# Optimization experiments

Measured on AMD Instinct MI355X. Metric: run time of the kernel, lower is better.

## Reference

```python
import jax, jax.numpy as jnp
import numpy as np

S = 72
IMG_W, IMG_H = 640, 360
STRIDE = 32
FMAP_H, FMAP_W = IMG_H // STRIDE, IMG_W // STRIDE  # 11, 20
N_OFFSETS = S
N_STRIPS = S - 1
ANGLES = np.array([15.0, 22.0, 30.0, 39.0, 49.0, 60.0, 72.0, 80.0, 90.0, 100.0, 108.0, 120.0, 131.0, 141.0, 150.0, 158.0, 165.0])
N_ANG = 17
N_PRED = 2 + 2 + 1 + N_OFFSETS  # 77
N_EDGE = FMAP_W + 2 * FMAP_H    # 42
N_PROP = N_ANG * N_EDGE         # 714
NMS_THRES = 15.0
BACKBONE_C = 512
CONV_C = 1024


def _make_anchors():
    anchor_ys = np.linspace(1.0, 0.0, N_OFFSETS)
    tan = np.tan(np.deg2rad(ANGLES))
    def side(origins):
        out = np.zeros((N_ANG, N_PRED, len(origins)), np.float32)
        for i, (sx, sy) in enumerate(origins):
            out[:, 2, i] = 1.0 - sy
            out[:, 3, i] = sx
            out[:, 5:, i] = (sx + (sy - anchor_ys)[None, :] / tan[:, None]) * IMG_W
        return out.reshape(N_ANG * N_PRED, len(origins))
    left = side([(0.0, y) for y in np.linspace(1.0, 0.0, FMAP_H)])
    right = side([(1.0, y) for y in np.linspace(1.0, 0.0, FMAP_H)])
    bottom = side([(x, 1.0) for x in np.linspace(1.0, 0.0, FMAP_W)])
    anchors = np.zeros((N_ANG * N_PRED, FMAP_H, FMAP_W), np.float32)
    anchors[:, :, 0] = left
    anchors[:, :, -1] = right
    anchors[:, -1, :] = bottom
    edge = np.concatenate([anchors[:, :, 0], anchors[:, :, -1], anchors[:, -1, :]], 1)  # [1309,42]
    anch_dim = edge.reshape(N_ANG, N_PRED, N_EDGE).transpose(2, 0, 1).reshape(N_PROP, N_PRED)
    return jnp.asarray(anchors), jnp.asarray(anch_dim)


def setup_inputs():
    key = jax.random.key(0)
    ks = jax.random.split(key, 4)
    B = 32
    feat = jax.random.normal(ks[0], (B, BACKBONE_C, FMAP_H, FMAP_W), jnp.float32)
    W_conv = jax.random.normal(ks[1], (CONV_C, BACKBONE_C), jnp.float32) * 0.02
    b_conv = jnp.zeros((CONV_C,), jnp.float32)
    W_cls = jax.random.normal(ks[2], (2 * N_ANG, CONV_C), jnp.float32) * 0.02
    b_cls = jnp.zeros((2 * N_ANG,), jnp.float32)
    W_reg = jax.random.normal(ks[3], (N_ANG * (N_OFFSETS + 1), CONV_C), jnp.float32) * 0.02
    b_reg = jnp.zeros((N_ANG * (N_OFFSETS + 1),), jnp.float32)
    anchors, anchors_anchor_dim = _make_anchors()
    return {"feat": feat, "W_conv": W_conv, "b_conv": b_conv, "W_cls": W_cls, "b_cls": b_cls,
            "W_reg": W_reg, "b_reg": b_reg, "anchors": anchors, "anchors_anchor_dim": anchors_anchor_dim}


def _proposals(feat, W_conv, b_conv, W_cls, b_cls, W_reg, b_reg, anchors):
    B = feat.shape[0]
    features = jnp.einsum('bchw,oc->bohw', feat, W_conv) + b_conv[None, :, None, None]
    cls_f = jnp.einsum('bchw,oc->bohw', features, W_cls) + b_cls[None, :, None, None]
    reg_f = jnp.einsum('bchw,oc->bohw', features, W_reg) + b_reg[None, :, None, None]
    anch = anchors.reshape(N_ANG, N_PRED, FMAP_H, FMAP_W)
    cls_r = cls_f.reshape(B, N_ANG, 2, FMAP_H, FMAP_W)
    reg_r = reg_f.reshape(B, N_ANG, N_OFFSETS + 1, FMAP_H, FMAP_W)
    # slots 0:2 <- cls logits (set), slots 2:4 <- anchor (copied), slots 4: <- anchor + reg
    mid = jnp.broadcast_to(anch[None, :, 2:4], (B, N_ANG, 2, FMAP_H, FMAP_W))
    tail = anch[None, :, 4:] + reg_r
    lane = jnp.concatenate([cls_r, mid, tail], axis=2)  # [B,17,77,h,w]
    # gather the three feature-map edges: left col, right col, bottom row
    edges = jnp.concatenate([lane[:, :, :, :, 0], lane[:, :, :, :, -1], lane[:, :, :, -1, :]], axis=3)  # [B,17,77,42]
    return edges.transpose(0, 3, 1, 2).reshape(B, N_PROP, N_PRED)  # [B,714,77]


def _nms_one(props, scores):
    # greedy line-NMS over proposals of one image, shapes static
    order = jnp.argsort(-scores)
    p = props[order]
    start = jnp.clip(jnp.round(p[:, 2] * N_STRIPS), 0.0, float(N_STRIPS))
    end = jnp.clip(start + p[:, 4] - 1.0, 0.0, float(N_STRIPS))
    xs = p[:, 5:]  # [N,72]
    s = jnp.maximum(start[:, None], start[None, :])
    e = jnp.minimum(end[:, None], end[None, :])
    idx = jnp.arange(N_OFFSETS, dtype=p.dtype)
    m = (idx[None, None, :] >= s[..., None]) & (idx[None, None, :] <= e[..., None])  # [N,N,72]
    diff = jnp.abs(xs[:, None, :] - xs[None, :, :])  # [N,N,72]
    cnt = e - s + 1.0
    dist = jnp.where(cnt > 0, jnp.sum(diff * m, -1) / jnp.maximum(cnt, 1.0), jnp.inf)
    sup = dist < NMS_THRES
    n = p.shape[0]
    pos = jnp.arange(n)
    def step(suppressed, i):
        keep_i = ~suppressed[i]
        suppressed = suppressed | (keep_i & sup[i] & (pos > i))
        return suppressed, keep_i
    _, keep_sorted = jax.lax.scan(step, jnp.zeros(n, bool), pos)
    return jnp.zeros(n, bool).at[order].set(keep_sorted)


def reference(feat, W_conv, b_conv, W_cls, b_cls, W_reg, b_reg, anchors, anchors_anchor_dim):
    proposals = _proposals(feat, W_conv, b_conv, W_cls, b_cls, W_reg, b_reg, anchors)
    scores = jax.nn.softmax(proposals[..., :2], axis=-1)[..., 1]  # [B,714]
    keep_mask = jax.lax.map(lambda pr: _nms_one(pr[0], pr[1]), (proposals, scores))  # [B,714]
    return proposals, keep_mask, scores
```

## Files before the change

kernel.cpp:

```cpp
#include <hip/hip_runtime.h>
#include <math.h>

#define NB     32
#define FH     11
#define FW     20
#define CIN    512
#define CMID   1024
#define NANG   17
#define NPREDD 77
#define NEDGE  42
#define NPROPP 714
#define NOFF   72
#define NCLS   34
#define NREGR  1241
#define N2PAD  1280
#define MTOT   1344
#define NSTRIPSF 71.0f
#define PADK   40

typedef unsigned long long u64;
typedef unsigned short ushortt;
typedef short s8v __attribute__((ext_vector_type(8)));
typedef ushortt u4v __attribute__((ext_vector_type(4)));
typedef float f4v __attribute__((ext_vector_type(4)));

__device__ inline ushortt f2bf(float f) {
    unsigned u = __float_as_uint(f);
    u += 0x7fffu + ((u >> 16) & 1u);
    return (ushortt)(u >> 16);
}
__device__ inline float bf2f(ushortt h) {
    return __uint_as_float(((unsigned)h) << 16);
}

__global__ __launch_bounds__(256) void k_prep(const float* __restrict__ feat,
                                              ushortt* __restrict__ A1hi,
                                              ushortt* __restrict__ A1lo,
                                              const float* __restrict__ Wconv,
                                              ushortt* __restrict__ B1h,
                                              ushortt* __restrict__ B1l,
                                              const float* __restrict__ Wcls,
                                              const float* __restrict__ Wreg,
                                              ushortt* __restrict__ B2h,
                                              ushortt* __restrict__ B2l,
                                              const float* __restrict__ AD,
                                              float* __restrict__ outP,
                                              float* __restrict__ kst)
{
    int bid = blockIdx.x, tid = threadIdx.x;
    if (bid < 2688) {
        int idx = bid * 256 + tid;
        int m = idx >> 9, c = idx & 511;
        int b = m / NEDGE, e = m - b * NEDGE;
        int h, w;
        if (e < FH)          { h = e;      w = 0;      }
        else if (e < 2 * FH) { h = e - FH; w = FW - 1; }
        else                 { h = FH - 1; w = e - 2 * FH; }
        float v = feat[((size_t)(b * CIN + c) * FH + h) * FW + w];
        ushortt hi = f2bf(v);
        A1hi[idx] = hi;
        A1lo[idx] = f2bf(v - bf2f(hi));
    } else if (bid < 2688 + 512) {
        int t = (bid - 2688) * 256 + tid;
        float4 v = *(const float4*)(Wconv + (size_t)t * 4);
        float vf[4] = {v.x, v.y, v.z, v.w};
        u4v hv, lv;
#pragma unroll
        for (int j = 0; j < 4; ++j) {
            ushortt h = f2bf(vf[j]);
            hv[j] = h;
            lv[j] = f2bf(vf[j] - bf2f(h));
        }
        *(u4v*)(B1h + (size_t)t * 4) = hv;
        *(u4v*)(B1l + (size_t)t * 4) = lv;
    } else if (bid < 4480) {
        int t = (bid - 3200) * 256 + tid;
        int row = t >> 8, col = (t & 255) * 4;
        float4 v = make_float4(0.f, 0.f, 0.f, 0.f);
        if (row < NCLS)              v = *(const float4*)(Wcls + (size_t)row * CMID + col);
        else if (row < NCLS + NREGR) v = *(const float4*)(Wreg + (size_t)(row - NCLS) * CMID + col);
        float vf[4] = {v.x, v.y, v.z, v.w};
        u4v hv, lv;
#pragma unroll
        for (int j = 0; j < 4; ++j) {
            ushortt h = f2bf(vf[j]);
            hv[j] = h;
            lv[j] = f2bf(vf[j] - bf2f(h));
        }
        *(u4v*)(B2h + (size_t)t * 4) = hv;
        *(u4v*)(B2l + (size_t)t * 4) = lv;
    } else if (bid < 4659) {
        int idx = (bid - 4480) * 256 + tid;
        if (idx < NB * NPROPP * 2) {
            int bp = idx >> 1;
            int p = 2 + (idx & 1);
            int prop = bp - (bp / NPROPP) * NPROPP;
            outP[(size_t)bp * NPREDD + p] = AD[prop * NPREDD + p];
        }
    } else {
        if (tid < NPROPP) {
            float p2 = AD[tid * NPREDD + 2];
            kst[tid] = fminf(fmaxf(rintf(p2 * NSTRIPSF), 0.0f), NSTRIPSF);
        }
    }
}

__global__ __launch_bounds__(256) void k_gemm1m(const ushortt* __restrict__ Ahi,
                                                const ushortt* __restrict__ Alo,
                                                const ushortt* __restrict__ Bh,
                                                const ushortt* __restrict__ Bl,
                                                const float* __restrict__ bias,
                                                ushortt* __restrict__ Chi,
                                                ushortt* __restrict__ Clo)
{
    const int K = CIN, N = CMID;
    __shared__ __align__(16) ushortt Ash[2][64 * PADK], Asl[2][64 * PADK];
    __shared__ __align__(16) ushortt Bsh[2][64 * PADK], Bsl[2][64 * PADK];
    int tid = threadIdx.x;
    int m0 = blockIdx.y * 64, n0 = blockIdx.x * 64;
    int srow = tid >> 2, sg = tid & 3;
    int lane = tid & 63, wv = tid >> 6;
    int wm = (wv & 1) * 32, wn = (wv >> 1) * 32;
    int quad = lane >> 4, l15 = lane & 15;
    int wo = srow * PADK + sg * 8;

    f4v acc[2][2];
#pragma unroll
    for (int i = 0; i < 2; ++i)
#pragma unroll
        for (int j = 0; j < 2; ++j) acc[i][j] = (f4v){0.f, 0.f, 0.f, 0.f};

    const ushortt* Ahp = Ahi + (size_t)(m0 + srow) * K + sg * 8;
    const ushortt* Alp = Alo + (size_t)(m0 + srow) * K + sg * 8;
    const ushortt* Bhp = Bh  + (size_t)(n0 + srow) * K + sg * 8;
    const ushortt* Blp = Bl  + (size_t)(n0 + srow) * K + sg * 8;

    s8v ra = *(const s8v*)Ahp;
    s8v rl = *(const s8v*)Alp;
    s8v rb = *(const s8v*)Bhp;
    s8v rc = *(const s8v*)Blp;
    *(s8v*)&Ash[0][wo] = ra;
    *(s8v*)&Asl[0][wo] = rl;
    *(s8v*)&Bsh[0][wo] = rb;
    *(s8v*)&Bsl[0][wo] = rc;
    __syncthreads();

    int buf = 0;
    for (int k0 = 0; k0 < K; k0 += 32) {
        bool more = (k0 + 32 < K);
        if (more) {
            ra = *(const s8v*)(Ahp + k0 + 32);
            rl = *(const s8v*)(Alp + k0 + 32);
            rb = *(const s8v*)(Bhp + k0 + 32);
            rc = *(const s8v*)(Blp + k0 + 32);
        }
        s8v ah[2], al[2], bh[2], bl[2];
#pragma unroll
        for (int s = 0; s < 2; ++s) {
            ah[s] = *(const s8v*)&Ash[buf][(wm + s * 16 + l15) * PADK + quad * 8];
            al[s] = *(const s8v*)&Asl[buf][(wm + s * 16 + l15) * PADK + quad * 8];
            bh[s] = *(const s8v*)&Bsh[buf][(wn + s * 16 + l15) * PADK + quad * 8];
            bl[s] = *(const s8v*)&Bsl[buf][(wn + s * 16 + l15) * PADK + quad * 8];
        }
#pragma unroll
        for (int sm = 0; sm < 2; ++sm)
#pragma unroll
            for (int sn = 0; sn < 2; ++sn) {
                acc[sm][sn] = __builtin_amdgcn_mfma_f32_16x16x32_bf16(al[sm], bh[sn], acc[sm][sn], 0, 0, 0);
                acc[sm][sn] = __builtin_amdgcn_mfma_f32_16x16x32_bf16(ah[sm], bl[sn], acc[sm][sn], 0, 0, 0);
                acc[sm][sn] = __builtin_amdgcn_mfma_f32_16x16x32_bf16(ah[sm], bh[sn], acc[sm][sn], 0, 0, 0);
            }
        if (more) {
            *(s8v*)&Ash[buf ^ 1][wo] = ra;
            *(s8v*)&Asl[buf ^ 1][wo] = rl;
            *(s8v*)&Bsh[buf ^ 1][wo] = rb;
            *(s8v*)&Bsl[buf ^ 1][wo] = rc;
        }
        __syncthreads();
        buf ^= 1;
    }
#pragma unroll
    for (int sm = 0; sm < 2; ++sm)
#pragma unroll
        for (int sn = 0; sn < 2; ++sn)
#pragma unroll
            for (int r = 0; r < 4; ++r) {
                int m = m0 + wm + sm * 16 + quad * 4 + r;
                int n = n0 + wn + sn * 16 + l15;
                float v = acc[sm][sn][r] + bias[n];
                ushortt h = f2bf(v);
                Chi[(size_t)m * N + n] = h;
                Clo[(size_t)m * N + n] = f2bf(v - bf2f(h));
            }
}

__global__ __launch_bounds__(256) void k_gemm2m(const ushortt* __restrict__ Ahi,
                                                const ushortt* __restrict__ Alo,
                                                const ushortt* __restrict__ Bh,
                                                const ushortt* __restrict__ Bl,
                                                const float* __restrict__ bcls,
                                                const float* __restrict__ breg,
                                                const float* __restrict__ AD,
                                                const float* __restrict__ kst,
                                                float* __restrict__ outP,
                                                float* __restrict__ outS,
                                                float* __restrict__ startv,
                                                float* __restrict__ endv,
                                                float* __restrict__ xsel)
{
    const int K = CMID;
    __shared__ __align__(16) ushortt Ash[2][64 * PADK], Asl[2][64 * PADK];
    __shared__ __align__(16) ushortt Bsh[2][64 * PADK], Bsl[2][64 * PADK];
    int tid = threadIdx.x;
    int m0 = blockIdx.y * 64, n0 = blockIdx.x * 64;
    int srow = tid >> 2, sg = tid & 3;
    int lane = tid & 63, wv = tid >> 6;
    int wm = (wv & 1) * 32, wn = (wv >> 1) * 32;
    int quad = lane >> 4, l15 = lane & 15;
    int wo = srow * PADK + sg * 8;

    f4v acc[2][2];
#pragma unroll
    for (int i = 0; i < 2; ++i)
#pragma unroll
        for (int j = 0; j < 2; ++j) acc[i][j] = (f4v){0.f, 0.f, 0.f, 0.f};

    const ushortt* Ahp = Ahi + (size_t)(m0 + srow) * K + sg * 8;
    const ushortt* Alp = Alo + (size_t)(m0 + srow) * K + sg * 8;
    const ushortt* Bhp = Bh  + (size_t)(n0 + srow) * K + sg * 8;
    const ushortt* Blp = Bl  + (size_t)(n0 + srow) * K + sg * 8;

    s8v ra = *(const s8v*)Ahp;
    s8v rl = *(const s8v*)Alp;
    s8v rb = *(const s8v*)Bhp;
    s8v rc = *(const s8v*)Blp;
    *(s8v*)&Ash[0][wo] = ra;
    *(s8v*)&Asl[0][wo] = rl;
    *(s8v*)&Bsh[0][wo] = rb;
    *(s8v*)&Bsl[0][wo] = rc;
    __syncthreads();

    int buf = 0;
    for (int k0 = 0; k0 < K; k0 += 32) {
        bool more = (k0 + 32 < K);
        if (more) {
            ra = *(const s8v*)(Ahp + k0 + 32);
            rl = *(const s8v*)(Alp + k0 + 32);
            rb = *(const s8v*)(Bhp + k0 + 32);
            rc = *(const s8v*)(Blp + k0 + 32);
        }
        s8v ah[2], al[2], bh[2], bl[2];
#pragma unroll
        for (int s = 0; s < 2; ++s) {
            ah[s] = *(const s8v*)&Ash[buf][(wm + s * 16 + l15) * PADK + quad * 8];
            al[s] = *(const s8v*)&Asl[buf][(wm + s * 16 + l15) * PADK + quad * 8];
            bh[s] = *(const s8v*)&Bsh[buf][(wn + s * 16 + l15) * PADK + quad * 8];
            bl[s] = *(const s8v*)&Bsl[buf][(wn + s * 16 + l15) * PADK + quad * 8];
        }
#pragma unroll
        for (int sm = 0; sm < 2; ++sm)
#pragma unroll
            for (int sn = 0; sn < 2; ++sn) {
                acc[sm][sn] = __builtin_amdgcn_mfma_f32_16x16x32_bf16(al[sm], bh[sn], acc[sm][sn], 0, 0, 0);
                acc[sm][sn] = __builtin_amdgcn_mfma_f32_16x16x32_bf16(ah[sm], bl[sn], acc[sm][sn], 0, 0, 0);
                acc[sm][sn] = __builtin_amdgcn_mfma_f32_16x16x32_bf16(ah[sm], bh[sn], acc[sm][sn], 0, 0, 0);
            }
        if (more) {
            *(s8v*)&Ash[buf ^ 1][wo] = ra;
            *(s8v*)&Asl[buf ^ 1][wo] = rl;
            *(s8v*)&Bsh[buf ^ 1][wo] = rb;
            *(s8v*)&Bsl[buf ^ 1][wo] = rc;
        }
        __syncthreads();
        buf ^= 1;
    }

#pragma unroll
    for (int sm = 0; sm < 2; ++sm)
#pragma unroll
        for (int sn = 0; sn < 2; ++sn)
#pragma unroll
            for (int r = 0; r < 4; ++r) {
                int m = m0 + wm + sm * 16 + quad * 4 + r;
                int n = n0 + wn + sn * 16 + l15;
                int b = m / NEDGE, e = m - b * NEDGE;
                bool isCls = (n < NCLS);
                bool isReg = (n >= NCLS) && (n < NCLS + NREGR);
                int q = n - NCLS;
                int a = isCls ? (n >> 1) : (q / 73);
                int p = isCls ? (n & 1) : (q - a * 73 + 4);
                int prop = e * NANG + a;
                float bb = isCls ? bcls[n] : (isReg ? breg[q] : 0.f);
                float t = acc[sm][sn][r] + bb;
                float tp = __shfl_xor(t, 1);
                float v = t;
                if (isReg) v = AD[(size_t)prop * NPREDD + p] + t;
                if (isCls || isReg)
                    outP[((size_t)b * NPROPP + prop) * NPREDD + p] = v;
                if (isCls && !(n & 1)) {
                    float mx = fmaxf(t, tp);
                    float e0 = expf(t - mx), e1 = expf(tp - mx);
                    outS[b * NPROPP + prop] = e1 / (e0 + e1);
                }
                if (isReg) {
                    float stf = kst[prop];
                    if (p == 4) {
                        float en = fminf(fmaxf(stf + v - 1.0f, 0.0f), NSTRIPSF);
                        startv[b * 720 + prop] = stf;
                        endv[b * 720 + prop] = en;
                    }
                    if (p == 5 + (int)stf)
                        xsel[b * 720 + prop] = v;
                }
            }
}

__global__ __launch_bounds__(128) void k_sort(const float* __restrict__ scores,
                                              int* __restrict__ order)
{
    int b = blockIdx.x, tile = blockIdx.y, tid = threadIdx.x;
    __shared__ __align__(16) float s[720];
    for (int x = tid; x < 720; x += 128)
        s[x] = (x < NPROPP) ? scores[b * NPROPP + x] : -1e30f;
    __syncthreads();
    int i = tile * 128 + tid;
    if (i >= NPROPP) return;
    float si = s[i];
    int r = 0;
#pragma unroll 4
    for (int j4 = 0; j4 < 720; j4 += 4) {
        float4 v = *(const float4*)&s[j4];
        r += (v.x > si) || (v.x == si && (j4 + 0) < i);
        r += (v.y > si) || (v.y == si && (j4 + 1) < i);
        r += (v.z > si) || (v.z == si && (j4 + 2) < i);
        r += (v.w > si) || (v.w == si && (j4 + 3) < i);
    }
    order[b * 720 + r] = i;
}

__global__ __launch_bounds__(256) void k_supmat(const float* __restrict__ outP,
                                                const float* __restrict__ startv,
                                                const float* __restrict__ endv,
                                                const float* __restrict__ xsel,
                                                const int* __restrict__ order,
                                                u64* __restrict__ sup)
{
    int jt = blockIdx.x, it = blockIdx.y, b = blockIdx.z;
    int i0 = it * 64, j0 = jt * 64;
    int tid = threadIdx.x;
    if (j0 + 63 < i0) {
        if (tid < 64) {
            int il = i0 + tid;
            if (il < NPROPP) sup[((size_t)b * NPROPP + il) * 12 + jt] = 0ull;
        }
        return;
    }
    __shared__ float SI[64], EI[64], XI[64];
    __shared__ float SJ[64], EJ[64], XJ[64];
    __shared__ int   OI[64], OJ[64];
    if (tid < 128) {
        int side = tid >> 6, q = tid & 63;
        int pos = (side ? j0 : i0) + q;
        int o = (pos < NPROPP) ? order[b * 720 + pos] : -1;
        float st = (o >= 0) ? startv[b * 720 + o] : 0.f;
        float en = (o >= 0) ? endv[b * 720 + o] : -2.f;
        float xv = (o >= 0) ? xsel[b * 720 + o] : 0.f;
        if (!side) { SI[q] = st; EI[q] = en; XI[q] = xv; OI[q] = o; }
        else       { SJ[q] = st; EJ[q] = en; XJ[q] = xv; OJ[q] = o; }
    }
    __syncthreads();
    int lane = tid & 63, w = tid >> 6;
    int j = j0 + lane;
    float sj = SJ[lane], ej = EJ[lane], xj = XJ[lane];
    const float* basexs = outP + (size_t)b * NPROPP * NPREDD + 5;
#pragma unroll 1
    for (int rep = 0; rep < 16; ++rep) {
        int iloc = w * 16 + rep;
        int il = i0 + iloc;
        float si = SI[iloc], ei = EI[iloc];
        float s = fmaxf(si, sj), e = fminf(ei, ej);
        float cnt = e - s + 1.0f;
        bool sp = false;
        if (cnt > 0.f) {
            if (e < s) {
                sp = true;
            } else {
                int ks = (int)s, ke = (int)e;
                if (si == sj && ke == ks) {
                    sp = (fabsf(XI[iloc] - xj) / fmaxf(cnt, 1.0f)) < 15.0f;
                } else {
                    const float* xi  = basexs + (size_t)OI[iloc] * NPREDD;
                    const float* xjp = basexs + (size_t)OJ[lane] * NPREDD;
                    float sum = 0.f;
                    for (int k = ks; k <= ke; ++k)
                        sum += fabsf(xi[k] - xjp[k]);
                    sp = (sum / fmaxf(cnt, 1.0f)) < 15.0f;
                }
            }
        }
        bool valid = (il < NPROPP) && (j < NPROPP) && (j > il);
        u64 msk = __ballot(valid && sp);
        if (lane == 0 && il < NPROPP)
            sup[((size_t)b * NPROPP + il) * 12 + jt] = msk;
    }
}

__global__ __launch_bounds__(256) void k_scan(const u64* __restrict__ sup,
                                              const int* __restrict__ order,
                                              float* __restrict__ keep_out)
{
    int b = blockIdx.x, tid = threadIdx.x;
    int lane = tid & 63;
    __shared__ u64 K[12], NS[12];
    __shared__ int changed;
    const u64* base = sup + (size_t)b * NPROPP * 12;

    int r0 = tid, r1 = tid + 256, r2 = tid + 512;
    u64 row0[12], row1[12], row2[12];
#pragma unroll
    for (int t = 0; t < 12; ++t) {
        row0[t] = base[(size_t)r0 * 12 + t];
        row1[t] = (r1 < NPROPP) ? base[(size_t)r1 * 12 + t] : 0ull;
        row2[t] = (r2 < NPROPP) ? base[(size_t)r2 * 12 + t] : 0ull;
    }
    if (tid < 12) {
        K[tid] = (tid < 11) ? ~0ull : ((1ull << (NPROPP - 704)) - 1ull);
        NS[tid] = 0ull;
    }
    __syncthreads();

    for (int sweep = 0; sweep < 720; ++sweep) {
        u64 m0 = 0ull - ((K[r0 >> 6] >> (r0 & 63)) & 1ull);
        u64 m1 = (r1 < NPROPP) ? (0ull - ((K[r1 >> 6] >> (r1 & 63)) & 1ull)) : 0ull;
        u64 m2 = (r2 < NPROPP) ? (0ull - ((K[r2 >> 6] >> (r2 & 63)) & 1ull)) : 0ull;
        unsigned lo[12], hi[12];
#pragma unroll
        for (int t = 0; t < 12; ++t) {
            u64 a = (row0[t] & m0) | (row1[t] & m1) | (row2[t] & m2);
            lo[t] = (unsigned)a;
            hi[t] = (unsigned)(a >> 32);
        }
#pragma unroll
        for (int s = 1; s < 64; s <<= 1) {
#pragma unroll
            for (int t = 0; t < 12; ++t) {
                lo[t] |= __shfl_xor(lo[t], s, 64);
                hi[t] |= __shfl_xor(hi[t], s, 64);
            }
        }
        if (tid == 0) changed = 0;
        if (lane == 0) {
#pragma unroll
            for (int t = 0; t < 12; ++t)
                atomicOr(&NS[t], ((u64)hi[t] << 32) | (u64)lo[t]);
        }
        __syncthreads();
        if (tid < 12) {
            u64 valid = (tid < 11) ? ~0ull : ((1ull << (NPROPP - 704)) - 1ull);
            u64 nk = valid & ~NS[tid];
            if (nk != K[tid]) changed = 1;
            K[tid] = nk;
            NS[tid] = 0ull;
        }
        __syncthreads();
        if (!changed) break;
    }
    if (r0 < NPROPP)
        keep_out[b * NPROPP + order[b * 720 + r0]] =
            ((K[r0 >> 6] >> (r0 & 63)) & 1ull) ? 1.f : 0.f;
    if (r1 < NPROPP)
        keep_out[b * NPROPP + order[b * 720 + r1]] =
            ((K[r1 >> 6] >> (r1 & 63)) & 1ull) ? 1.f : 0.f;
    if (r2 < NPROPP)
        keep_out[b * NPROPP + order[b * 720 + r2]] =
            ((K[r2 >> 6] >> (r2 & 63)) & 1ull) ? 1.f : 0.f;
}

extern "C" void kernel_launch(void* const* d_in, const int* in_sizes, int n_in,
                              void* d_out, int out_size, void* d_ws, size_t ws_size,
                              hipStream_t stream)
{
    const float* feat  = (const float*)d_in[0];
    const float* Wconv = (const float*)d_in[1];
    const float* bconv = (const float*)d_in[2];
    const float* Wcls  = (const float*)d_in[3];
    const float* bcls  = (const float*)d_in[4];
    const float* Wreg  = (const float*)d_in[5];
    const float* breg  = (const float*)d_in[6];
    const float* AD    = (const float*)d_in[8];

    float* out  = (float*)d_out;
    float* outP = out;
    float* outK = out + (size_t)NB * NPROPP * NPREDD;
    float* outS = outK + (size_t)NB * NPROPP;

    float* ws = (float*)d_ws;
    ushortt* A1hi = (ushortt*)ws;
    ushortt* A1lo = (ushortt*)(ws + 344064);
    ushortt* A2hi = (ushortt*)(ws + 688128);
    ushortt* A2lo = (ushortt*)(ws + 1376256);
    float*   kst  = ws + 2064384;
    ushortt* B1h  = (ushortt*)(ws + 3784704);
    ushortt* B1l  = (ushortt*)(ws + 4046848);
    ushortt* B2h  = (ushortt*)(ws + 4308992);
    ushortt* B2l  = (ushortt*)(ws + 4964352);
    float* startv = ws;
    float* endv   = ws + 23040;
    int*   order  = (int*)(ws + 46080);
    u64*   sup    = (u64*)(ws + 69120);
    float* xsel   = ws + 617472;

    k_prep        <<<dim3(4660),       dim3(256), 0, stream>>>(feat, A1hi, A1lo,
                                                               Wconv, B1h, B1l,
                                                               Wcls, Wreg, B2h, B2l,
                                                               AD, outP, kst);
    k_gemm1m      <<<dim3(16, 21),     dim3(256), 0, stream>>>(A1hi, A1lo, B1h, B1l, bconv, A2hi, A2lo);
    k_gemm2m      <<<dim3(20, 21),     dim3(256), 0, stream>>>(A2hi, A2lo, B2h, B2l, bcls, breg,
                                                               AD, kst, outP, outS, startv, endv, xsel);
    k_sort        <<<dim3(NB, 6),      dim3(128), 0, stream>>>(outS, order);
    k_supmat      <<<dim3(12, 12, NB), dim3(256), 0, stream>>>(outP, startv, endv, xsel, order, sup);
    k_scan        <<<dim3(NB),         dim3(256), 0, stream>>>(sup, order, outK);
}
```

Baseline: 201.3 us.

## Stage feature planes through shared memory and add lo*lo MFMA term

The feature gather in the prep kernel now has each block load 32 full contiguous channel planes into shared memory, split them into bf16 hi/lo pairs, and then write only the 42 edge positions. This replaces the earlier strided per-element gather across the feature map, which was poorly coalesced, with contiguous reads, at the cost of reading the whole plane rather than only the edge pixels. Both GEMMs also gain an extra lo*lo MFMA per tile, adding a fourth bf16 product for accuracy and increasing MFMA work by a third. The grid shrinks to match the new block partitioning.

```diff
diff --git a/kernel.cpp b/kernel.cpp
--- a/kernel.cpp
+++ b/kernel.cpp
@@ -47,21 +47,33 @@
                                               float* __restrict__ outP,
                                               float* __restrict__ kst)
 {
+    __shared__ unsigned T[32 * 221];
     int bid = blockIdx.x, tid = threadIdx.x;
-    if (bid < 2688) {
-        int idx = bid * 256 + tid;
-        int m = idx >> 9, c = idx & 511;
-        int b = m / NEDGE, e = m - b * NEDGE;
-        int h, w;
-        if (e < FH)          { h = e;      w = 0;      }
-        else if (e < 2 * FH) { h = e - FH; w = FW - 1; }
-        else                 { h = FH - 1; w = e - 2 * FH; }
-        float v = feat[((size_t)(b * CIN + c) * FH + h) * FW + w];
-        ushortt hi = f2bf(v);
-        A1hi[idx] = hi;
-        A1lo[idx] = f2bf(v - bf2f(hi));
-    } else if (bid < 2688 + 512) {
-        int t = (bid - 2688) * 256 + tid;
+    if (bid < 512) {
+        int p0 = bid * 32;
+        int b  = p0 >> 9;
+        int c0 = p0 & 511;
+        const float* fp = feat + (size_t)p0 * 220;
+        for (int i = tid; i < 32 * 220; i += 256) {
+            float v = fp[i];
+            int pl = i / 220, off = i - pl * 220;
+            ushortt hi = f2bf(v);
+            ushortt lo = f2bf(v - bf2f(hi));
+            T[pl * 221 + off] = ((unsigned)hi) | (((unsigned)lo) << 16);
+        }
+        __syncthreads();
+        int cl = tid & 31;
+        for (int e = tid >> 5; e < NEDGE; e += 8) {
+            int hw = (e < FH) ? e * FW
+                   : (e < 2 * FH) ? (e - FH) * FW + (FW - 1)
+                   : (FH - 1) * FW + (e - 2 * FH);
+            unsigned u = T[cl * 221 + hw];
+            size_t o = (size_t)(b * NEDGE + e) * CIN + c0 + cl;
+            A1hi[o] = (ushortt)(u & 0xffffu);
+            A1lo[o] = (ushortt)(u >> 16);
+        }
+    } else if (bid < 1024) {
+        int t = (bid - 512) * 256 + tid;
         float4 v = *(const float4*)(Wconv + (size_t)t * 4);
         float vf[4] = {v.x, v.y, v.z, v.w};
         u4v hv, lv;
@@ -73,8 +85,8 @@
         }
         *(u4v*)(B1h + (size_t)t * 4) = hv;
         *(u4v*)(B1l + (size_t)t * 4) = lv;
-    } else if (bid < 4480) {
-        int t = (bid - 3200) * 256 + tid;
+    } else if (bid < 2304) {
+        int t = (bid - 1024) * 256 + tid;
         int row = t >> 8, col = (t & 255) * 4;
         float4 v = make_float4(0.f, 0.f, 0.f, 0.f);
         if (row < NCLS)              v = *(const float4*)(Wcls + (size_t)row * CMID + col);
@@ -89,8 +101,8 @@
         }
         *(u4v*)(B2h + (size_t)t * 4) = hv;
         *(u4v*)(B2l + (size_t)t * 4) = lv;
-    } else if (bid < 4659) {
-        int idx = (bid - 4480) * 256 + tid;
+    } else if (bid < 2483) {
+        int idx = (bid - 2304) * 256 + tid;
         if (idx < NB * NPROPP * 2) {
             int bp = idx >> 1;
             int p = 2 + (idx & 1);
@@ -166,6 +178,7 @@
         for (int sm = 0; sm < 2; ++sm)
 #pragma unroll
             for (int sn = 0; sn < 2; ++sn) {
+                acc[sm][sn] = __builtin_amdgcn_mfma_f32_16x16x32_bf16(al[sm], bl[sn], acc[sm][sn], 0, 0, 0);
                 acc[sm][sn] = __builtin_amdgcn_mfma_f32_16x16x32_bf16(al[sm], bh[sn], acc[sm][sn], 0, 0, 0);
                 acc[sm][sn] = __builtin_amdgcn_mfma_f32_16x16x32_bf16(ah[sm], bl[sn], acc[sm][sn], 0, 0, 0);
                 acc[sm][sn] = __builtin_amdgcn_mfma_f32_16x16x32_bf16(ah[sm], bh[sn], acc[sm][sn], 0, 0, 0);
@@ -261,6 +274,7 @@
         for (int sm = 0; sm < 2; ++sm)
 #pragma unroll
             for (int sn = 0; sn < 2; ++sn) {
+                acc[sm][sn] = __builtin_amdgcn_mfma_f32_16x16x32_bf16(al[sm], bl[sn], acc[sm][sn], 0, 0, 0);
                 acc[sm][sn] = __builtin_amdgcn_mfma_f32_16x16x32_bf16(al[sm], bh[sn], acc[sm][sn], 0, 0, 0);
                 acc[sm][sn] = __builtin_amdgcn_mfma_f32_16x16x32_bf16(ah[sm], bl[sn], acc[sm][sn], 0, 0, 0);
                 acc[sm][sn] = __builtin_amdgcn_mfma_f32_16x16x32_bf16(ah[sm], bh[sn], acc[sm][sn], 0, 0, 0);
@@ -510,7 +524,7 @@
     u64*   sup    = (u64*)(ws + 69120);
     float* xsel   = ws + 617472;
 
-    k_prep        <<<dim3(4660),       dim3(256), 0, stream>>>(feat, A1hi, A1lo,
+    k_prep        <<<dim3(2484),       dim3(256), 0, stream>>>(feat, A1hi, A1lo,
                                                                Wconv, B1h, B1l,
                                                                Wcls, Wreg, B2h, B2l,
                                                                AD, outP, kst);
```

After: 201.6 us. No clear change (+0.2%).
